# Kernel tuning notes

Hardware: AMD Instinct MI355X
Metric: run time of the kernel (lower is better)

The kernel has to match this reference:

```python
import jax, jax.numpy as jnp
import numpy as np

POS_THR = 0.5      # ROI_POSITIVE_THR
NEG_THR = 0.1      # ROI_NEGATIVE_THR
N_SAMPLES = 256    # ROI_SAMPLES
FG_RATIO = 0.25    # ROI_SAMPLE_RATIO
L1W = 1.0          # RPN.L1WEIGHT_INTERSECTION
NUM_FG = int(N_SAMPLES * FG_RATIO)


def _make_boxes(kxy, kwh, shape):
    # valid [x1,y1,x2,y2] boxes in an ~800px image
    xy = jax.random.uniform(kxy, shape[:-1] + (2,)) * 800.0
    wh = jax.random.uniform(kwh, shape[:-1] + (2,)) * 200.0 + 1.0
    return jnp.concatenate([xy, xy + wh], axis=-1)


def setup_inputs() -> dict:
    key = jax.random.key(0)
    k1, k2, k3, k4 = jax.random.split(key, 4)
    proposals = _make_boxes(k1, k2, (16, 16384, 4))  # [B, N, 4]
    gt_boxes = _make_boxes(k3, k4, (16, 128, 4))     # [B, G, 4]
    return {"proposals": proposals, "gt_boxes": gt_boxes}


def _centrehw(b):
    # [x1,y1,x2,y2] -> [cx,cy,w,h]
    x1, y1, x2, y2 = b[..., 0], b[..., 1], b[..., 2], b[..., 3]
    return jnp.stack([(x1 + x2) * 0.5, (y1 + y2) * 0.5, x2 - x1, y2 - y1], axis=-1)


def _targets(gt_c, roi_c):
    dx = (gt_c[..., 0] - roi_c[..., 0]) / roi_c[..., 2]
    dy = (gt_c[..., 1] - roi_c[..., 1]) / roi_c[..., 3]
    dw = jnp.log(gt_c[..., 2] / roi_c[..., 2])
    dh = jnp.log(gt_c[..., 3] / roi_c[..., 3])
    return jnp.stack([dx, dy, dw, dh], axis=-1)


def _iou(prop, gt):
    # prop [B,N,4], gt [B,G,4] -> IoU [B,N,G]
    p = prop[:, :, None, :]
    g = gt[:, None, :, :]
    ix1 = jnp.maximum(p[..., 0], g[..., 0])
    iy1 = jnp.maximum(p[..., 1], g[..., 1])
    ix2 = jnp.minimum(p[..., 2], g[..., 2])
    iy2 = jnp.minimum(p[..., 3], g[..., 3])
    inter = jnp.clip(ix2 - ix1, 0.0) * jnp.clip(iy2 - iy1, 0.0)
    ap = (p[..., 2] - p[..., 0]) * (p[..., 3] - p[..., 1])
    ag = (g[..., 2] - g[..., 0]) * (g[..., 3] - g[..., 1])
    return inter / jnp.maximum(ap + ag - inter, 1e-8)


def _forward(proposals, gt_boxes):
    B, N, _ = proposals.shape
    iou = _iou(proposals, gt_boxes)                       # [B,N,G]
    max_iou = iou.max(axis=-1)                            # [B,N]
    argmax_gt = iou.argmax(axis=-1).astype(jnp.int32)     # [B,N]
    # classify: 1=fg, 0=bg, -1=ignore
    labels = jnp.where(max_iou >= POS_THR, 1,
                       jnp.where(max_iou < NEG_THR, 0, -1)).astype(jnp.int32)
    # randsample: keep <= NUM_FG positives (random), fill rest with negatives.
    r = jax.random.uniform(jax.random.key(1), (B, N))
    pos = labels == 1
    r_pos = jnp.where(pos, r, -1.0)
    order = jnp.argsort(-r_pos, axis=1)
    ranks = jnp.argsort(order, axis=1)                    # rank among positives by r
    pos_sel = pos & (ranks < NUM_FG)
    prio = jnp.where(pos_sel, 3.0 + r,
                     jnp.where(labels == 0, 2.0 + r,
                               jnp.where(pos, 1.0 + r, r)))
    _, idx = jax.lax.top_k(prio, N_SAMPLES)               # [B,S] sampled proposal ids
    batch_labels = jnp.maximum(jnp.take_along_axis(labels, idx, axis=1), 0)  # [B,S]
    roi_batch = jnp.take_along_axis(proposals, idx[..., None], axis=1)       # [B,S,4]
    sel_gt = jnp.take_along_axis(argmax_gt, idx, axis=1)                     # [B,S]
    gt_batch = jnp.take_along_axis(gt_boxes, sel_gt[..., None], axis=1)      # [B,S,4]
    bbox_targets = _targets(_centrehw(gt_batch), _centrehw(roi_batch))       # [B,S,4]
    in_w = jnp.where((batch_labels == 1)[..., None], L1W, 0.0)
    in_w = jnp.broadcast_to(in_w, bbox_targets.shape)
    out_w = (in_w > 0).astype(jnp.float32)
    return roi_batch, batch_labels, bbox_targets, in_w, out_w


def reference(proposals, gt_boxes):
    return _forward(proposals, gt_boxes)
```

## Files before the change

kernel.cpp:

```cpp
#include <hip/hip_runtime.h>
#include <stdint.h>

#define BATCH 16
#define NPROP 16384
#define NGT   128
#define NSAMP 256
#define NFG   64
#define GCAP  512
#define CSTR  128
#define NEGT  0x780002u

typedef unsigned long long ull;

__device__ __forceinline__ void thr_block(uint32_t c0, uint32_t c1,
                                          uint32_t* o0, uint32_t* o1) {
    const uint32_t k0 = 0u, k1 = 1u, ks2 = 0x1BD11BDBu;
    uint32_t x0 = c0 + k0, x1 = c1 + k1;
#define RND(d) { x0 += x1; x1 = (x1 << d) | (x1 >> (32 - d)); x1 ^= x0; }
    RND(13) RND(15) RND(26) RND(6)   x0 += k1;  x1 += ks2 + 1u;
    RND(17) RND(29) RND(16) RND(24)  x0 += ks2; x1 += k0 + 2u;
    RND(13) RND(15) RND(26) RND(6)   x0 += k0;  x1 += k1 + 3u;
    RND(17) RND(29) RND(16) RND(24)  x0 += k1;  x1 += ks2 + 4u;
    RND(13) RND(15) RND(26) RND(6)   x0 += ks2; x1 += k0 + 5u;
#undef RND
    *o0 = x0; *o1 = x1;
}

__device__ __forceinline__ uint32_t thr_part_xor(uint32_t f) {
    uint32_t a, b; thr_block(0u, f, &a, &b);
    return a ^ b;
}

__global__ void k_zero(uint32_t* c) {
    for (int i = threadIdx.x; i < BATCH * CSTR; i += 1024) c[i] = 0u;
}

__global__ void __launch_bounds__(256) k_compute(
    const float* __restrict__ props, const float* __restrict__ gts,
    ull* __restrict__ lists, uint32_t* __restrict__ cnts)
{
#pragma clang fp contract(off)
    const int b = blockIdx.y;
    const int tid = threadIdx.x;
    const int half = tid & 1;
    const int n = blockIdx.x * 128 + (tid >> 1);
    __shared__ float2 sA[130];
    __shared__ float2 sB[130];
    __shared__ float  sag[130];
    __shared__ uint32_t wc[4][4];
    __shared__ uint32_t we[4][4];
    __shared__ uint32_t sBase[4];
    if (tid < NGT) {
        float4 g = ((const float4*)gts)[(size_t)b * NGT + tid];
        int idx = (tid < 64) ? tid : tid + 1;
        sA[idx] = make_float2(g.x, g.y);
        sB[idx] = make_float2(g.z, g.w);
        sag[idx] = (g.z - g.x) * (g.w - g.y);
    }
    __syncthreads();
    const float4 pb = ((const float4*)props)[(size_t)b * NPROP + n];
    const float ap = (pb.z - pb.x) * (pb.w - pb.y);
    float best = -1.0f; int bg = 0;
    const int base  = half ? 65 : 0;
    const int gbias = half ? 64 : 0;
    #pragma unroll 4
    for (int i = 0; i < 64; ++i) {
        const float2 a = sA[base + i];
        const float2 c = sB[base + i];
        float w  = fmaxf(fminf(pb.z, c.x) - fmaxf(pb.x, a.x), 0.0f);
        float hh = fmaxf(fminf(pb.w, c.y) - fmaxf(pb.y, a.y), 0.0f);
        float inter = w * hh;
        float un = fmaxf(ap + sag[base + i] - inter, 1e-8f);
        float iou = inter / un;
        if (iou > best) { best = iou; bg = gbias + i; }
    }
    float ob = __shfl_xor(best, 1);
    int  obg = __shfl_xor(bg, 1);
    if (half == 0 && ob > best) { best = ob; bg = obg; }

    uint32_t lab = (best >= 0.5f) ? 2u : ((best < 0.1f) ? 1u : 0u);
    const uint32_t f = (uint32_t)b * NPROP + (uint32_t)n;
    uint32_t mant = thr_part_xor(f) >> 9;
    ull entry = ((ull)(lab == 2u) << 44) | ((ull)mant << 21)
              | ((ull)(16383u - (uint32_t)n) << 7) | (ull)(uint32_t)bg;

    const bool isEven = (half == 0);
    bool cP = isEven && (lab == 2u);
    bool cH = isEven && (lab == 1u) && (mant >= NEGT);
    bool cL = isEven && (lab == 1u) && (mant <  NEGT);
    bool cI = isEven && (lab == 0u);
    ull mP = __ballot(cP), mH = __ballot(cH), mL = __ballot(cL), mI = __ballot(cI);
    const int w = tid >> 6;
    const uint32_t lane = (uint32_t)tid & 63u;
    if (lane == 0) {
        wc[0][w] = (uint32_t)__popcll(mP);
        wc[1][w] = (uint32_t)__popcll(mH);
        wc[2][w] = (uint32_t)__popcll(mL);
        wc[3][w] = (uint32_t)__popcll(mI);
    }
    __syncthreads();
    if (tid < 4) {
        uint32_t e = 0;
        #pragma unroll
        for (int i = 0; i < 4; i++) { we[tid][i] = e; e += wc[tid][i]; }
        sBase[tid] = e ? atomicAdd(&cnts[b * CSTR + tid * 32], e) : 0u;
    }
    __syncthreads();
    ull lt = lane ? (~0ull >> (64u - lane)) : 0ull;
    ull* slab = lists + ((size_t)b * 4) * NPROP;
    if (cP) slab[0 * NPROP + sBase[0] + we[0][w] + (uint32_t)__popcll(mP & lt)] = entry;
    if (cH) slab[1 * NPROP + sBase[1] + we[1][w] + (uint32_t)__popcll(mH & lt)] = entry;
    if (cL) slab[2 * NPROP + sBase[2] + we[2][w] + (uint32_t)__popcll(mL & lt)] = entry;
    if (cI) slab[3 * NPROP + sBase[3] + we[3][w] + (uint32_t)__popcll(mI & lt)] = entry;
}

__global__ void __launch_bounds__(1024) k_select(
    const float* __restrict__ props, const float* __restrict__ gts,
    const ull* __restrict__ lists, const uint32_t* __restrict__ cnts,
    float* __restrict__ out)
{
#pragma clang fp contract(off)
    const int b = blockIdx.x;
    const int tid = threadIdx.x;
    __shared__ uint32_t hist[2048];
    __shared__ ull      gat[GCAP];
    __shared__ ull      selk[NSAMP];
    __shared__ uint32_t sela[NSAMP];
    __shared__ uint32_t sh_dig, sh_k, sh_cnt_in, gcnt, selc;
    __shared__ ull sh_thr;

    const ull* Ppos  = lists + ((size_t)b * 4 + 0) * NPROP;
    const ull* PnegH = lists + ((size_t)b * 4 + 1) * NPROP;
    const ull* PnegL = lists + ((size_t)b * 4 + 2) * NPROP;
    const ull* Pign  = lists + ((size_t)b * 4 + 3) * NPROP;
    const uint32_t npos = cnts[b * CSTR + 0];
    const uint32_t nH   = cnts[b * CSTR + 32];
    const uint32_t nL   = cnts[b * CSTR + 64];
    const uint32_t nig  = cnts[b * CSTR + 96];
    const uint32_t nneg = nH + nL;
    const uint32_t npn  = npos + nneg;
    if (tid == 0) selc = 0;
    __syncthreads();

    auto keyA_of = [](ull e) -> ull {
        return (((e >> 21) & 0x7FFFFFull) << 14) | ((e >> 7) & 0x3FFFull);
    };

    auto locate = [&](uint32_t k) {
        if (tid < 64) {
            const uint32_t lane = (uint32_t)tid;
            uint32_t cs = 0;
            if (lane < 32) {
                const uint32_t base = lane * 64u;
                #pragma unroll 8
                for (uint32_t i = 0; i < 64; i++) cs += hist[base + i];
            }
            uint32_t s = cs;
            #pragma unroll
            for (int off = 1; off < 32; off <<= 1) {
                uint32_t t = __shfl_down(s, off);
                if (lane + off < 32) s += t;
            }
            uint32_t sExcl = s - cs;
            bool cond = (lane < 32) && (sExcl < k) && (k <= s);
            ull ball = __ballot(cond);
            uint32_t cstar = (uint32_t)(__ffsll((unsigned long long)ball) - 1);
            uint32_t kc = (uint32_t)__shfl((int)(k - sExcl), (int)cstar);
            uint32_t val = hist[cstar * 64u + lane];
            uint32_t fi = val;
            #pragma unroll
            for (int off = 1; off < 64; off <<= 1) {
                uint32_t t = __shfl_down(fi, off);
                if (lane + off < 64) fi += t;
            }
            uint32_t fExcl = fi - val;
            bool cond2 = (fExcl < kc) && (kc <= fi);
            ull ball2 = __ballot(cond2);
            uint32_t bstar = (uint32_t)(__ffsll((unsigned long long)ball2) - 1);
            if (lane == bstar) {
                sh_dig = cstar * 64u + lane;
                sh_k = kc - fExcl;
                sh_cnt_in = val;
            }
        }
    };

    auto radix = [&](auto&& kf, uint32_t m, uint32_t k, int shift) -> ull {
        if (m <= GCAP) {
            if (tid == 0) gcnt = 0;
            __syncthreads();
            for (uint32_t j = tid; j < m; j += 1024) {
                bool e; ull key = kf(j, e);
                if (e) { uint32_t s = atomicAdd(&gcnt, 1u); gat[s] = key; }
            }
            __syncthreads();
            uint32_t gc = gcnt;
            if (tid < (int)gc) {
                ull x = gat[tid];
                uint32_t r = 0;
                for (uint32_t j = 0; j < gc; j++) r += (gat[j] > x);
                if (r == k - 1) sh_thr = x;
            }
            __syncthreads();
            return sh_thr;
        }
        ull prefix = 0, mask = 0;
        for (;;) {
            hist[tid] = 0; hist[tid + 1024] = 0;
            __syncthreads();
            for (uint32_t j = tid; j < m; j += 1024) {
                bool e; ull key = kf(j, e);
                if (e && ((key ^ prefix) & mask) == 0)
                    atomicAdd(&hist[(uint32_t)(key >> shift) & 2047u], 1u);
            }
            __syncthreads();
            locate(k);
            __syncthreads();
            uint32_t dig = sh_dig, kk = sh_k, cnt = sh_cnt_in;
            prefix |= ((ull)dig) << shift;
            mask   |= 2047ull << shift;
            if (cnt <= GCAP || shift == 0) {
                if (tid == 0) gcnt = 0;
                __syncthreads();
                for (uint32_t j = tid; j < m; j += 1024) {
                    bool e; ull key = kf(j, e);
                    if (e && ((key ^ prefix) & mask) == 0) {
                        uint32_t s = atomicAdd(&gcnt, 1u);
                        if (s < GCAP) gat[s] = key;
                    }
                }
                __syncthreads();
                uint32_t gc = (gcnt < GCAP) ? gcnt : GCAP;
                if (tid < (int)gc) {
                    ull x = gat[tid];
                    uint32_t r = 0;
                    for (uint32_t j = 0; j < gc; j++) r += (gat[j] > x);
                    if (r == kk - 1) sh_thr = x;
                }
                __syncthreads();
                return sh_thr;
            } else {
                k = kk;
                shift = (shift >= 11) ? shift - 11 : 0;
                __syncthreads();
            }
        }
    };

    ull thrA = 0;
    if (npos > NFG) {
        thrA = radix([&](uint32_t j, bool& e) -> ull {
            e = true; return keyA_of(Ppos[j]); }, npos, NFG, 26);
    }

    auto keyB_pos = [&](ull ent) -> ull {
        uint32_t mant = (uint32_t)((ent >> 21) & 0x7FFFFFull);
        uint32_t invn = (uint32_t)((ent >> 7) & 0x3FFFull);
        float r = __uint_as_float(0x3F800000u | mant) - 1.0f;
        uint32_t cls = (keyA_of(ent) >= thrA) ? 3u : 1u;
        float prio = (float)cls + r;
        return (((ull)__float_as_uint(prio)) << 14) | (ull)invn;
    };
    auto keyB_neg = [](ull ent) -> ull {
        uint32_t mant = (uint32_t)((ent >> 21) & 0x7FFFFFull);
        uint32_t invn = (uint32_t)((ent >> 7) & 0x3FFFull);
        float r = __uint_as_float(0x3F800000u | mant) - 1.0f;
        float prio = 2.0f + r;
        return (((ull)__float_as_uint(prio)) << 14) | (ull)invn;
    };
    auto keyB_ign = [](ull ent) -> ull {
        uint32_t mant = (uint32_t)((ent >> 21) & 0x7FFFFFull);
        uint32_t invn = (uint32_t)((ent >> 7) & 0x3FFFull);
        float r = __uint_as_float(0x3F800000u | mant) - 1.0f;
        float prio = 0.0f + r;
        return (((ull)__float_as_uint(prio)) << 14) | (ull)invn;
    };

    const uint32_t c3 = (npos < NFG) ? npos : NFG;
    const uint32_t c2 = nneg;
    uint32_t clsStar = (npn >= NSAMP) ? ((NSAMP <= c3 + c2) ? 2u : 1u) : 0u;
    bool scanL = true;
    const bool scanI = (clsStar == 0u);
    ull thrB = 0;
    if (clsStar == 2u) {
        uint32_t k2 = NSAMP - c3;
        if (nH >= k2) {
            scanL = false;
            thrB = radix([&](uint32_t j, bool& e) -> ull {
                e = true; return keyB_neg(PnegH[j]); }, nH, k2, 25);
        } else {
            thrB = radix([&](uint32_t j, bool& e) -> ull {
                e = true; return keyB_neg(j < nH ? PnegH[j] : PnegL[j - nH]); },
                nneg, k2, 25);
        }
    } else if (clsStar == 1u) {
        uint32_t k1 = NSAMP - c3 - c2;
        thrB = radix([&](uint32_t j, bool& e) -> ull {
            ull kb = keyB_pos(Ppos[j]);
            e = ((kb >> 14) < 0x40000000ull);
            return kb; }, npos, k1, 26);
    } else {
        uint32_t k0 = NSAMP - npn;
        thrB = radix([&](uint32_t j, bool& e) -> ull {
            e = true; return keyB_ign(Pign[j]); }, nig, k0, 34);
    }
    __syncthreads();

    auto push = [&](ull key, ull ent, uint32_t fg) {
        uint32_t s = atomicAdd(&selc, 1u);
        if (s < NSAMP) { selk[s] = key; sela[s] = (fg << 7) | (uint32_t)(ent & 0x7Full); }
    };
    for (uint32_t j = tid; j < npos; j += 1024) {
        ull ent = Ppos[j]; ull key = keyB_pos(ent);
        if (clsStar == 0u || key >= thrB) push(key, ent, 1u);
    }
    for (uint32_t j = tid; j < nH; j += 1024) {
        ull ent = PnegH[j]; ull key = keyB_neg(ent);
        if (clsStar == 0u || key >= thrB) push(key, ent, 0u);
    }
    if (scanL) {
        for (uint32_t j = tid; j < nL; j += 1024) {
            ull ent = PnegL[j]; ull key = keyB_neg(ent);
            if (clsStar == 0u || key >= thrB) push(key, ent, 0u);
        }
    }
    if (scanI) {
        for (uint32_t j = tid; j < nig; j += 1024) {
            ull ent = Pign[j]; ull key = keyB_ign(ent);
            if (key >= thrB) push(key, ent, 0u);
        }
    }
    __syncthreads();

    if (tid < NSAMP) {
        ull x = selk[tid];
        uint32_t r = 0;
        for (int j = 0; j < NSAMP; j++) r += (selk[j] > x);
        uint32_t n = 16383u - (uint32_t)((x >> 0) & 0x3FFFull);
        uint32_t aux = sela[tid];
        uint32_t bg = aux & 0x7Fu;
        const int isfg = (int)((aux >> 7) & 1u);
        const float4 pb = ((const float4*)props)[(size_t)b * NPROP + n];
        const float4 gb = ((const float4*)gts)[(size_t)b * NGT + bg];
        const size_t O_ROI = 0;
        const size_t O_LBL = (size_t)BATCH * NSAMP * 4;
        const size_t O_TGT = O_LBL + (size_t)BATCH * NSAMP;
        const size_t O_INW = O_TGT + (size_t)BATCH * NSAMP * 4;
        const size_t O_OUW = O_INW + (size_t)BATCH * NSAMP * 4;
        const size_t row = (size_t)b * NSAMP + r;
        out[O_ROI + row * 4 + 0] = pb.x;
        out[O_ROI + row * 4 + 1] = pb.y;
        out[O_ROI + row * 4 + 2] = pb.z;
        out[O_ROI + row * 4 + 3] = pb.w;
        out[O_LBL + row] = isfg ? 1.0f : 0.0f;
        float rw  = pb.z - pb.x, rh = pb.w - pb.y;
        float gw  = gb.z - gb.x, gh = gb.w - gb.y;
        out[O_TGT + row * 4 + 0] = ((gb.x + gb.z) * 0.5f - (pb.x + pb.z) * 0.5f) / rw;
        out[O_TGT + row * 4 + 1] = ((gb.y + gb.w) * 0.5f - (pb.y + pb.w) * 0.5f) / rh;
        out[O_TGT + row * 4 + 2] = logf(gw / rw);
        out[O_TGT + row * 4 + 3] = logf(gh / rh);
        float wv = isfg ? 1.0f : 0.0f;
        for (int c = 0; c < 4; c++) {
            out[O_INW + row * 4 + c] = wv;
            out[O_OUW + row * 4 + c] = wv;
        }
    }
}

extern "C" void kernel_launch(void* const* d_in, const int* in_sizes, int n_in,
                              void* d_out, int out_size, void* d_ws, size_t ws_size,
                              hipStream_t stream) {
    (void)in_sizes; (void)n_in; (void)out_size; (void)ws_size;
    const float* props = (const float*)d_in[0];
    const float* gts   = (const float*)d_in[1];
    ull* lists = (ull*)d_ws;
    uint32_t* cnts = (uint32_t*)((char*)d_ws + (size_t)BATCH * 4 * NPROP * 8);
    float* out = (float*)d_out;

    k_zero<<<1, 1024, 0, stream>>>(cnts);
    dim3 gridA(NPROP / 128, BATCH);
    k_compute<<<gridA, 256, 0, stream>>>(props, gts, lists, cnts);
    k_select<<<BATCH, 1024, 0, stream>>>(props, gts, lists, cnts, out);
}
```

Before: 96.23 us.

## Skip non-overlapping IoU divisions, use per-block segments instead of global atomics

```diff
diff --git a/kernel.cpp b/kernel.cpp
--- a/kernel.cpp
+++ b/kernel.cpp
@@ -7,8 +7,10 @@
 #define NSAMP 256
 #define NFG   64
 #define GCAP  512
-#define CSTR  128
-#define NEGT  0x780002u
+#define PCAP  8192
+#define NCAP  4096
+#define NBLK  128
+#define BPB   128
 
 typedef unsigned long long ull;
 
@@ -31,25 +33,20 @@
     return a ^ b;
 }
 
-__global__ void k_zero(uint32_t* c) {
-    for (int i = threadIdx.x; i < BATCH * CSTR; i += 1024) c[i] = 0u;
-}
-
 __global__ void __launch_bounds__(256) k_compute(
     const float* __restrict__ props, const float* __restrict__ gts,
-    ull* __restrict__ lists, uint32_t* __restrict__ cnts)
+    ull* __restrict__ lists, uint32_t* __restrict__ cntblk)
 {
 #pragma clang fp contract(off)
     const int b = blockIdx.y;
+    const int blk = blockIdx.x;
     const int tid = threadIdx.x;
     const int half = tid & 1;
-    const int n = blockIdx.x * 128 + (tid >> 1);
+    const int n = blk * BPB + (tid >> 1);
     __shared__ float2 sA[130];
     __shared__ float2 sB[130];
     __shared__ float  sag[130];
-    __shared__ uint32_t wc[4][4];
-    __shared__ uint32_t we[4][4];
-    __shared__ uint32_t sBase[4];
+    __shared__ uint32_t wc[3][4], we_s[3][4];
     if (tid < NGT) {
         float4 g = ((const float4*)gts)[(size_t)b * NGT + tid];
         int idx = (tid < 64) ? tid : tid + 1;
@@ -60,11 +57,30 @@
     __syncthreads();
     const float4 pb = ((const float4*)props)[(size_t)b * NPROP + n];
     const float ap = (pb.z - pb.x) * (pb.w - pb.y);
-    float best = -1.0f; int bg = 0;
     const int base  = half ? 65 : 0;
     const int gbias = half ? 64 : 0;
+
+    uint32_t m0 = 0, m1 = 0;
     #pragma unroll 4
-    for (int i = 0; i < 64; ++i) {
+    for (int i = 0; i < 32; ++i) {
+        const float2 a = sA[base + i];
+        const float2 c = sB[base + i];
+        uint32_t hit = (fminf(pb.z, c.x) > fmaxf(pb.x, a.x)) &
+                       (fminf(pb.w, c.y) > fmaxf(pb.y, a.y));
+        m0 |= hit << i;
+    }
+    #pragma unroll 4
+    for (int i = 0; i < 32; ++i) {
+        const float2 a = sA[base + 32 + i];
+        const float2 c = sB[base + 32 + i];
+        uint32_t hit = (fminf(pb.z, c.x) > fmaxf(pb.x, a.x)) &
+                       (fminf(pb.w, c.y) > fmaxf(pb.y, a.y));
+        m1 |= hit << i;
+    }
+
+    float best = 0.0f; int bg = gbias;
+    while (m0) {
+        int i = __builtin_ctz(m0); m0 &= m0 - 1;
         const float2 a = sA[base + i];
         const float2 c = sB[base + i];
         float w  = fmaxf(fminf(pb.z, c.x) - fmaxf(pb.x, a.x), 0.0f);
@@ -74,6 +90,18 @@
         float iou = inter / un;
         if (iou > best) { best = iou; bg = gbias + i; }
     }
+    while (m1) {
+        int i = 32 + __builtin_ctz(m1); m1 &= m1 - 1;
+        const float2 a = sA[base + i];
+        const float2 c = sB[base + i];
+        float w  = fmaxf(fminf(pb.z, c.x) - fmaxf(pb.x, a.x), 0.0f);
+        float hh = fmaxf(fminf(pb.w, c.y) - fmaxf(pb.y, a.y), 0.0f);
+        float inter = w * hh;
+        float un = fmaxf(ap + sag[base + i] - inter, 1e-8f);
+        float iou = inter / un;
+        if (iou > best) { best = iou; bg = gbias + i; }
+    }
+
     float ob = __shfl_xor(best, 1);
     int  obg = __shfl_xor(bg, 1);
     if (half == 0 && ob > best) { best = ob; bg = obg; }
@@ -86,61 +114,90 @@
 
     const bool isEven = (half == 0);
     bool cP = isEven && (lab == 2u);
-    bool cH = isEven && (lab == 1u) && (mant >= NEGT);
-    bool cL = isEven && (lab == 1u) && (mant <  NEGT);
+    bool cN = isEven && (lab == 1u);
     bool cI = isEven && (lab == 0u);
-    ull mP = __ballot(cP), mH = __ballot(cH), mL = __ballot(cL), mI = __ballot(cI);
+    ull mP = __ballot(cP), mN = __ballot(cN), mI = __ballot(cI);
     const int w = tid >> 6;
     const uint32_t lane = (uint32_t)tid & 63u;
     if (lane == 0) {
         wc[0][w] = (uint32_t)__popcll(mP);
-        wc[1][w] = (uint32_t)__popcll(mH);
-        wc[2][w] = (uint32_t)__popcll(mL);
-        wc[3][w] = (uint32_t)__popcll(mI);
-    }
-    __syncthreads();
-    if (tid < 4) {
+        wc[1][w] = (uint32_t)__popcll(mN);
+        wc[2][w] = (uint32_t)__popcll(mI);
+    }
+    __syncthreads();
+    if (tid < 3) {
         uint32_t e = 0;
         #pragma unroll
-        for (int i = 0; i < 4; i++) { we[tid][i] = e; e += wc[tid][i]; }
-        sBase[tid] = e ? atomicAdd(&cnts[b * CSTR + tid * 32], e) : 0u;
+        for (int i = 0; i < 4; i++) { we_s[tid][i] = e; e += wc[tid][i]; }
+        cntblk[((size_t)b * NBLK + blk) * 4 + tid] = e;
     }
     __syncthreads();
     ull lt = lane ? (~0ull >> (64u - lane)) : 0ull;
-    ull* slab = lists + ((size_t)b * 4) * NPROP;
-    if (cP) slab[0 * NPROP + sBase[0] + we[0][w] + (uint32_t)__popcll(mP & lt)] = entry;
-    if (cH) slab[1 * NPROP + sBase[1] + we[1][w] + (uint32_t)__popcll(mH & lt)] = entry;
-    if (cL) slab[2 * NPROP + sBase[2] + we[2][w] + (uint32_t)__popcll(mL & lt)] = entry;
-    if (cI) slab[3 * NPROP + sBase[3] + we[3][w] + (uint32_t)__popcll(mI & lt)] = entry;
+    ull* slab = lists + (size_t)b * 3 * NPROP;
+    const uint32_t segB = (uint32_t)blk * BPB;
+    if (cP) slab[0 * NPROP + segB + we_s[0][w] + (uint32_t)__popcll(mP & lt)] = entry;
+    if (cN) slab[1 * NPROP + segB + we_s[1][w] + (uint32_t)__popcll(mN & lt)] = entry;
+    if (cI) slab[2 * NPROP + segB + we_s[2][w] + (uint32_t)__popcll(mI & lt)] = entry;
 }
 
 __global__ void __launch_bounds__(1024) k_select(
     const float* __restrict__ props, const float* __restrict__ gts,
-    const ull* __restrict__ lists, const uint32_t* __restrict__ cnts,
+    const ull* __restrict__ lists, const uint32_t* __restrict__ cntblk,
     float* __restrict__ out)
 {
 #pragma clang fp contract(off)
     const int b = blockIdx.x;
     const int tid = threadIdx.x;
+    __shared__ ull      dpos[PCAP];
+    __shared__ ull      dneg[NCAP];
     __shared__ uint32_t hist[2048];
     __shared__ ull      gat[GCAP];
     __shared__ ull      selk[NSAMP];
     __shared__ uint32_t sela[NSAMP];
+    __shared__ uint32_t bc[NBLK * 4];
+    __shared__ uint32_t preP[NBLK], preN[NBLK];
     __shared__ uint32_t sh_dig, sh_k, sh_cnt_in, gcnt, selc;
+    __shared__ uint32_t totP, totN, totI;
     __shared__ ull sh_thr;
 
-    const ull* Ppos  = lists + ((size_t)b * 4 + 0) * NPROP;
-    const ull* PnegH = lists + ((size_t)b * 4 + 1) * NPROP;
-    const ull* PnegL = lists + ((size_t)b * 4 + 2) * NPROP;
-    const ull* Pign  = lists + ((size_t)b * 4 + 3) * NPROP;
-    const uint32_t npos = cnts[b * CSTR + 0];
-    const uint32_t nH   = cnts[b * CSTR + 32];
-    const uint32_t nL   = cnts[b * CSTR + 64];
-    const uint32_t nig  = cnts[b * CSTR + 96];
-    const uint32_t nneg = nH + nL;
-    const uint32_t npn  = npos + nneg;
+    const ull* Spos = lists + (size_t)b * 3 * NPROP;
+    const ull* Sneg = Spos + NPROP;
+    const ull* Sign = Sneg + NPROP;
+    if (tid < NBLK * 4) bc[tid] = cntblk[(size_t)b * NBLK * 4 + tid];
     if (tid == 0) selc = 0;
     __syncthreads();
+    if (tid < 3) {
+        uint32_t run = 0;
+        for (int blk = 0; blk < NBLK; ++blk) {
+            uint32_t v = bc[blk * 4 + tid];
+            if (tid == 0) preP[blk] = run;
+            else if (tid == 1) preN[blk] = run;
+            run += v;
+        }
+        if (tid == 0) totP = run; else if (tid == 1) totN = run; else totI = run;
+    }
+    __syncthreads();
+    const uint32_t npos = totP, nneg = totN, nig = totI;
+    const bool posL = (npos <= PCAP), negL = (nneg <= NCAP);
+    for (uint32_t s = tid; s < NPROP; s += 1024) {
+        uint32_t blk = s >> 7, i = s & 127u;
+        if (posL && i < bc[blk * 4 + 0]) dpos[preP[blk] + i] = Spos[s];
+        if (negL && i < bc[blk * 4 + 1]) dneg[preN[blk] + i] = Sneg[s];
+    }
+    __syncthreads();
+
+    const uint32_t mPos = posL ? npos : NPROP;
+    const uint32_t mNeg = negL ? nneg : NPROP;
+    auto posEnt = [&](uint32_t j, bool& e) -> ull {
+        if (posL) { e = true; return dpos[j]; }
+        e = (j & 127u) < bc[(j >> 7) * 4 + 0];
+        return e ? Spos[j] : 0ull;
+    };
+    auto negEnt = [&](uint32_t j, bool& e) -> ull {
+        if (negL) { e = true; return dneg[j]; }
+        e = (j & 127u) < bc[(j >> 7) * 4 + 1];
+        return e ? Sneg[j] : 0ull;
+    };
 
     auto keyA_of = [](ull e) -> ull {
         return (((e >> 21) & 0x7FFFFFull) << 14) | ((e >> 7) & 0x3FFFull);
@@ -250,7 +307,7 @@
     ull thrA = 0;
     if (npos > NFG) {
         thrA = radix([&](uint32_t j, bool& e) -> ull {
-            e = true; return keyA_of(Ppos[j]); }, npos, NFG, 26);
+            ull ent = posEnt(j, e); return keyA_of(ent); }, mPos, NFG, 26);
     }
 
     auto keyB_pos = [&](ull ent) -> ull {
@@ -278,31 +335,22 @@
 
     const uint32_t c3 = (npos < NFG) ? npos : NFG;
     const uint32_t c2 = nneg;
+    const uint32_t npn = npos + nneg;
     uint32_t clsStar = (npn >= NSAMP) ? ((NSAMP <= c3 + c2) ? 2u : 1u) : 0u;
-    bool scanL = true;
-    const bool scanI = (clsStar == 0u);
     ull thrB = 0;
     if (clsStar == 2u) {
-        uint32_t k2 = NSAMP - c3;
-        if (nH >= k2) {
-            scanL = false;
-            thrB = radix([&](uint32_t j, bool& e) -> ull {
-                e = true; return keyB_neg(PnegH[j]); }, nH, k2, 25);
-        } else {
-            thrB = radix([&](uint32_t j, bool& e) -> ull {
-                e = true; return keyB_neg(j < nH ? PnegH[j] : PnegL[j - nH]); },
-                nneg, k2, 25);
-        }
+        thrB = radix([&](uint32_t j, bool& e) -> ull {
+            ull ent = negEnt(j, e); return keyB_neg(ent); }, mNeg, NSAMP - c3, 26);
     } else if (clsStar == 1u) {
-        uint32_t k1 = NSAMP - c3 - c2;
         thrB = radix([&](uint32_t j, bool& e) -> ull {
-            ull kb = keyB_pos(Ppos[j]);
-            e = ((kb >> 14) < 0x40000000ull);
-            return kb; }, npos, k1, 26);
+            ull ent = posEnt(j, e);
+            ull kb = keyB_pos(ent);
+            e = e && ((kb >> 14) < 0x40000000ull);
+            return kb; }, mPos, NSAMP - c3 - c2, 26);
     } else {
-        uint32_t k0 = NSAMP - npn;
         thrB = radix([&](uint32_t j, bool& e) -> ull {
-            e = true; return keyB_ign(Pign[j]); }, nig, k0, 34);
+            e = (j & 127u) < bc[(j >> 7) * 4 + 2];
+            return e ? keyB_ign(Sign[j]) : 0ull; }, NPROP, NSAMP - npn, 34);
     }
     __syncthreads();
 
@@ -310,24 +358,25 @@
         uint32_t s = atomicAdd(&selc, 1u);
         if (s < NSAMP) { selk[s] = key; sela[s] = (fg << 7) | (uint32_t)(ent & 0x7Full); }
     };
-    for (uint32_t j = tid; j < npos; j += 1024) {
-        ull ent = Ppos[j]; ull key = keyB_pos(ent);
+    for (uint32_t j = tid; j < mPos; j += 1024) {
+        bool e; ull ent = posEnt(j, e);
+        if (!e) continue;
+        ull key = keyB_pos(ent);
         if (clsStar == 0u || key >= thrB) push(key, ent, 1u);
     }
-    for (uint32_t j = tid; j < nH; j += 1024) {
-        ull ent = PnegH[j]; ull key = keyB_neg(ent);
+    for (uint32_t j = tid; j < mNeg; j += 1024) {
+        bool e; ull ent = negEnt(j, e);
+        if (!e) continue;
+        ull key = keyB_neg(ent);
         if (clsStar == 0u || key >= thrB) push(key, ent, 0u);
     }
-    if (scanL) {
-        for (uint32_t j = tid; j < nL; j += 1024) {
-            ull ent = PnegL[j]; ull key = keyB_neg(ent);
-            if (clsStar == 0u || key >= thrB) push(key, ent, 0u);
-        }
-    }
-    if (scanI) {
-        for (uint32_t j = tid; j < nig; j += 1024) {
-            ull ent = Pign[j]; ull key = keyB_ign(ent);
-            if (key >= thrB) push(key, ent, 0u);
+    if (clsStar == 0u) {
+        for (uint32_t j = tid; j < NPROP; j += 1024) {
+            if (((j & 127u) < bc[(j >> 7) * 4 + 2])) {
+                ull ent = Sign[j];
+                ull key = keyB_ign(ent);
+                if (key >= thrB) push(key, ent, 0u);
+            }
         }
     }
     __syncthreads();
@@ -336,7 +385,7 @@
         ull x = selk[tid];
         uint32_t r = 0;
         for (int j = 0; j < NSAMP; j++) r += (selk[j] > x);
-        uint32_t n = 16383u - (uint32_t)((x >> 0) & 0x3FFFull);
+        uint32_t n = 16383u - (uint32_t)(x & 0x3FFFull);
         uint32_t aux = sela[tid];
         uint32_t bg = aux & 0x7Fu;
         const int isfg = (int)((aux >> 7) & 1u);
@@ -374,11 +423,10 @@
     const float* props = (const float*)d_in[0];
     const float* gts   = (const float*)d_in[1];
     ull* lists = (ull*)d_ws;
-    uint32_t* cnts = (uint32_t*)((char*)d_ws + (size_t)BATCH * 4 * NPROP * 8);
+    uint32_t* cntblk = (uint32_t*)((char*)d_ws + (size_t)BATCH * 3 * NPROP * 8);
     float* out = (float*)d_out;
 
-    k_zero<<<1, 1024, 0, stream>>>(cnts);
-    dim3 gridA(NPROP / 128, BATCH);
-    k_compute<<<gridA, 256, 0, stream>>>(props, gts, lists, cnts);
-    k_select<<<BATCH, 1024, 0, stream>>>(props, gts, lists, cnts, out);
+    dim3 gridA(NPROP / BPB, BATCH);
+    k_compute<<<gridA, 256, 0, stream>>>(props, gts, lists, cntblk);
+    k_select<<<BATCH, 1024, 0, stream>>>(props, gts, lists, cntblk, out);
 }
```

Result: slower. 109.4 us (+13.7%).

## Fuse IoU/bucketing and selection into one persistent kernel with grid barrier

Applied to the files above, without the earlier changes.

```diff
diff --git a/kernel.cpp b/kernel.cpp
--- a/kernel.cpp
+++ b/kernel.cpp
@@ -7,7 +7,7 @@
 #define NSAMP 256
 #define NFG   64
 #define GCAP  512
-#define CSTR  128
+#define PCAP  8192
 #define NEGT  0x780002u
 
 typedef unsigned long long ull;
@@ -31,97 +31,25 @@
     return a ^ b;
 }
 
-__global__ void k_zero(uint32_t* c) {
-    for (int i = threadIdx.x; i < BATCH * CSTR; i += 1024) c[i] = 0u;
+__global__ void k_init(uint32_t* z) {
+    if (threadIdx.x < 16 * 8 * 2 + 2) z[threadIdx.x] = 0u;
 }
 
-__global__ void __launch_bounds__(256) k_compute(
+__global__ void __launch_bounds__(1024, 4) k_fused(
     const float* __restrict__ props, const float* __restrict__ gts,
-    ull* __restrict__ lists, uint32_t* __restrict__ cnts)
+    ull* __restrict__ lists, ull* __restrict__ cnts, uint32_t* __restrict__ bar,
+    float* __restrict__ out)
 {
 #pragma clang fp contract(off)
-    const int b = blockIdx.y;
     const int tid = threadIdx.x;
-    const int half = tid & 1;
-    const int n = blockIdx.x * 128 + (tid >> 1);
+    const int bid = blockIdx.x;
+
     __shared__ float2 sA[130];
     __shared__ float2 sB[130];
     __shared__ float  sag[130];
-    __shared__ uint32_t wc[4][4];
-    __shared__ uint32_t we[4][4];
-    __shared__ uint32_t sBase[4];
-    if (tid < NGT) {
-        float4 g = ((const float4*)gts)[(size_t)b * NGT + tid];
-        int idx = (tid < 64) ? tid : tid + 1;
-        sA[idx] = make_float2(g.x, g.y);
-        sB[idx] = make_float2(g.z, g.w);
-        sag[idx] = (g.z - g.x) * (g.w - g.y);
-    }
-    __syncthreads();
-    const float4 pb = ((const float4*)props)[(size_t)b * NPROP + n];
-    const float ap = (pb.z - pb.x) * (pb.w - pb.y);
-    float best = -1.0f; int bg = 0;
-    const int base  = half ? 65 : 0;
-    const int gbias = half ? 64 : 0;
-    #pragma unroll 4
-    for (int i = 0; i < 64; ++i) {
-        const float2 a = sA[base + i];
-        const float2 c = sB[base + i];
-        float w  = fmaxf(fminf(pb.z, c.x) - fmaxf(pb.x, a.x), 0.0f);
-        float hh = fmaxf(fminf(pb.w, c.y) - fmaxf(pb.y, a.y), 0.0f);
-        float inter = w * hh;
-        float un = fmaxf(ap + sag[base + i] - inter, 1e-8f);
-        float iou = inter / un;
-        if (iou > best) { best = iou; bg = gbias + i; }
-    }
-    float ob = __shfl_xor(best, 1);
-    int  obg = __shfl_xor(bg, 1);
-    if (half == 0 && ob > best) { best = ob; bg = obg; }
-
-    uint32_t lab = (best >= 0.5f) ? 2u : ((best < 0.1f) ? 1u : 0u);
-    const uint32_t f = (uint32_t)b * NPROP + (uint32_t)n;
-    uint32_t mant = thr_part_xor(f) >> 9;
-    ull entry = ((ull)(lab == 2u) << 44) | ((ull)mant << 21)
-              | ((ull)(16383u - (uint32_t)n) << 7) | (ull)(uint32_t)bg;
-
-    const bool isEven = (half == 0);
-    bool cP = isEven && (lab == 2u);
-    bool cH = isEven && (lab == 1u) && (mant >= NEGT);
-    bool cL = isEven && (lab == 1u) && (mant <  NEGT);
-    bool cI = isEven && (lab == 0u);
-    ull mP = __ballot(cP), mH = __ballot(cH), mL = __ballot(cL), mI = __ballot(cI);
-    const int w = tid >> 6;
-    const uint32_t lane = (uint32_t)tid & 63u;
-    if (lane == 0) {
-        wc[0][w] = (uint32_t)__popcll(mP);
-        wc[1][w] = (uint32_t)__popcll(mH);
-        wc[2][w] = (uint32_t)__popcll(mL);
-        wc[3][w] = (uint32_t)__popcll(mI);
-    }
-    __syncthreads();
-    if (tid < 4) {
-        uint32_t e = 0;
-        #pragma unroll
-        for (int i = 0; i < 4; i++) { we[tid][i] = e; e += wc[tid][i]; }
-        sBase[tid] = e ? atomicAdd(&cnts[b * CSTR + tid * 32], e) : 0u;
-    }
-    __syncthreads();
-    ull lt = lane ? (~0ull >> (64u - lane)) : 0ull;
-    ull* slab = lists + ((size_t)b * 4) * NPROP;
-    if (cP) slab[0 * NPROP + sBase[0] + we[0][w] + (uint32_t)__popcll(mP & lt)] = entry;
-    if (cH) slab[1 * NPROP + sBase[1] + we[1][w] + (uint32_t)__popcll(mH & lt)] = entry;
-    if (cL) slab[2 * NPROP + sBase[2] + we[2][w] + (uint32_t)__popcll(mL & lt)] = entry;
-    if (cI) slab[3 * NPROP + sBase[3] + we[3][w] + (uint32_t)__popcll(mI & lt)] = entry;
-}
-
-__global__ void __launch_bounds__(1024) k_select(
-    const float* __restrict__ props, const float* __restrict__ gts,
-    const ull* __restrict__ lists, const uint32_t* __restrict__ cnts,
-    float* __restrict__ out)
-{
-#pragma clang fp contract(off)
-    const int b = blockIdx.x;
-    const int tid = threadIdx.x;
+    __shared__ uint32_t wc[4][16], we_s[4][16];
+    __shared__ ull sPack;
+    __shared__ ull      dpos[PCAP];
     __shared__ uint32_t hist[2048];
     __shared__ ull      gat[GCAP];
     __shared__ ull      selk[NSAMP];
@@ -129,19 +57,123 @@
     __shared__ uint32_t sh_dig, sh_k, sh_cnt_in, gcnt, selc;
     __shared__ ull sh_thr;
 
-    const ull* Ppos  = lists + ((size_t)b * 4 + 0) * NPROP;
-    const ull* PnegH = lists + ((size_t)b * 4 + 1) * NPROP;
-    const ull* PnegL = lists + ((size_t)b * 4 + 2) * NPROP;
-    const ull* Pign  = lists + ((size_t)b * 4 + 3) * NPROP;
-    const uint32_t npos = cnts[b * CSTR + 0];
-    const uint32_t nH   = cnts[b * CSTR + 32];
-    const uint32_t nL   = cnts[b * CSTR + 64];
-    const uint32_t nig  = cnts[b * CSTR + 96];
+    {
+        const int ab = bid >> 4;
+        const int half = tid & 1;
+        if (tid < NGT) {
+            float4 g = ((const float4*)gts)[(size_t)ab * NGT + tid];
+            int idx = (tid < 64) ? tid : tid + 1;
+            sA[idx] = make_float2(g.x, g.y);
+            sB[idx] = make_float2(g.z, g.w);
+            sag[idx] = (g.z - g.x) * (g.w - g.y);
+        }
+        __syncthreads();
+        const int base  = half ? 65 : 0;
+        const int gbias = half ? 64 : 0;
+        ull* slab = lists + (size_t)ab * 4 * NPROP;
+
+        for (int cc = 0; cc < 2; ++cc) {
+            const int seg = (bid & 15) * 2 + cc;
+            const int n = seg * 512 + (tid >> 1);
+            const float4 pb = ((const float4*)props)[(size_t)ab * NPROP + n];
+            const float ap = (pb.z - pb.x) * (pb.w - pb.y);
+            float best = -1.0f; int bg = 0;
+            #pragma unroll 4
+            for (int i = 0; i < 64; ++i) {
+                const float2 a = sA[base + i];
+                const float2 c = sB[base + i];
+                float w  = fmaxf(fminf(pb.z, c.x) - fmaxf(pb.x, a.x), 0.0f);
+                float hh = fmaxf(fminf(pb.w, c.y) - fmaxf(pb.y, a.y), 0.0f);
+                float inter = w * hh;
+                float un = fmaxf(ap + sag[base + i] - inter, 1e-8f);
+                float iou = inter / un;
+                if (iou > best) { best = iou; bg = gbias + i; }
+            }
+            float ob = __shfl_xor(best, 1);
+            int  obg = __shfl_xor(bg, 1);
+            if (half == 0 && ob > best) { best = ob; bg = obg; }
+
+            uint32_t lab = (best >= 0.5f) ? 2u : ((best < 0.1f) ? 1u : 0u);
+            const uint32_t f = (uint32_t)ab * NPROP + (uint32_t)n;
+            uint32_t mant = thr_part_xor(f) >> 9;
+            ull entry = ((ull)(lab == 2u) << 44) | ((ull)mant << 21)
+                      | ((ull)(16383u - (uint32_t)n) << 7) | (ull)(uint32_t)bg;
+
+            const bool isEven = (half == 0);
+            bool cP = isEven && (lab == 2u);
+            bool cH = isEven && (lab == 1u) && (mant >= NEGT);
+            bool cL = isEven && (lab == 1u) && (mant <  NEGT);
+            bool cI = isEven && (lab == 0u);
+            ull mP = __ballot(cP), mH = __ballot(cH), mL = __ballot(cL), mI = __ballot(cI);
+            const int w = tid >> 6;
+            const uint32_t lane = (uint32_t)tid & 63u;
+            if (lane == 0) {
+                wc[0][w] = (uint32_t)__popcll(mP);
+                wc[1][w] = (uint32_t)__popcll(mH);
+                wc[2][w] = (uint32_t)__popcll(mL);
+                wc[3][w] = (uint32_t)__popcll(mI);
+            }
+            __syncthreads();
+            if (tid < 4) {
+                uint32_t e = 0;
+                #pragma unroll
+                for (int i = 0; i < 16; i++) { we_s[tid][i] = e; e += wc[tid][i]; }
+                uint32_t e0 = (uint32_t)__shfl((int)e, 0);
+                uint32_t e1 = (uint32_t)__shfl((int)e, 1);
+                uint32_t e2 = (uint32_t)__shfl((int)e, 2);
+                uint32_t e3 = (uint32_t)__shfl((int)e, 3);
+                if (tid == 0) {
+                    ull add = (ull)e0 | ((ull)e1 << 16) | ((ull)e2 << 32) | ((ull)e3 << 48);
+                    sPack = atomicAdd(&cnts[(size_t)ab * 8], add);
+                }
+            }
+            __syncthreads();
+            ull pk = sPack;
+            uint32_t b0 = (uint32_t)(pk)       & 0xFFFFu;
+            uint32_t b1 = (uint32_t)(pk >> 16) & 0xFFFFu;
+            uint32_t b2 = (uint32_t)(pk >> 32) & 0xFFFFu;
+            uint32_t b3 = (uint32_t)(pk >> 48) & 0xFFFFu;
+            ull lt = lane ? (~0ull >> (64u - lane)) : 0ull;
+            if (cP) slab[0 * NPROP + b0 + we_s[0][w] + (uint32_t)__popcll(mP & lt)] = entry;
+            if (cH) slab[1 * NPROP + b1 + we_s[1][w] + (uint32_t)__popcll(mH & lt)] = entry;
+            if (cL) slab[2 * NPROP + b2 + we_s[2][w] + (uint32_t)__popcll(mL & lt)] = entry;
+            if (cI) slab[3 * NPROP + b3 + we_s[3][w] + (uint32_t)__popcll(mI & lt)] = entry;
+            __syncthreads();
+        }
+    }
+
+    __syncthreads();
+    if (tid == 0) {
+        __threadfence();
+        uint32_t arrived = atomicAdd(&bar[0], 1u) + 1u;
+        if (arrived == (uint32_t)gridDim.x) {
+            atomicExch(&bar[1], 1u);
+        } else {
+            while (atomicAdd(&bar[1], 0u) == 0u) __builtin_amdgcn_s_sleep(8);
+        }
+        __threadfence();
+    }
+    __syncthreads();
+    if (bid >= BATCH) return;
+
+    const int sb = bid;
+    const ull* Ppos  = lists + ((size_t)sb * 4 + 0) * NPROP;
+    const ull* PnegH = lists + ((size_t)sb * 4 + 1) * NPROP;
+    const ull* PnegL = lists + ((size_t)sb * 4 + 2) * NPROP;
+    const ull* Pign  = lists + ((size_t)sb * 4 + 3) * NPROP;
+    const ull pk = cnts[(size_t)sb * 8];
+    const uint32_t npos = (uint32_t)(pk)       & 0xFFFFu;
+    const uint32_t nH   = (uint32_t)(pk >> 16) & 0xFFFFu;
+    const uint32_t nL   = (uint32_t)(pk >> 32) & 0xFFFFu;
+    const uint32_t nig  = (uint32_t)(pk >> 48) & 0xFFFFu;
     const uint32_t nneg = nH + nL;
     const uint32_t npn  = npos + nneg;
+    const bool inP = (npos <= PCAP);
     if (tid == 0) selc = 0;
+    if (inP) for (uint32_t j = tid; j < npos; j += 1024) dpos[j] = Ppos[j];
     __syncthreads();
 
+    auto posEnt = [&](uint32_t j) -> ull { return inP ? dpos[j] : Ppos[j]; };
     auto keyA_of = [](ull e) -> ull {
         return (((e >> 21) & 0x7FFFFFull) << 14) | ((e >> 7) & 0x3FFFull);
     };
@@ -250,7 +282,7 @@
     ull thrA = 0;
     if (npos > NFG) {
         thrA = radix([&](uint32_t j, bool& e) -> ull {
-            e = true; return keyA_of(Ppos[j]); }, npos, NFG, 26);
+            e = true; return keyA_of(posEnt(j)); }, npos, NFG, 26);
     }
 
     auto keyB_pos = [&](ull ent) -> ull {
@@ -287,22 +319,20 @@
         if (nH >= k2) {
             scanL = false;
             thrB = radix([&](uint32_t j, bool& e) -> ull {
-                e = true; return keyB_neg(PnegH[j]); }, nH, k2, 25);
+                e = true; return keyB_neg(PnegH[j]); }, nH, k2, 26);
         } else {
             thrB = radix([&](uint32_t j, bool& e) -> ull {
                 e = true; return keyB_neg(j < nH ? PnegH[j] : PnegL[j - nH]); },
-                nneg, k2, 25);
+                nneg, k2, 26);
         }
     } else if (clsStar == 1u) {
-        uint32_t k1 = NSAMP - c3 - c2;
         thrB = radix([&](uint32_t j, bool& e) -> ull {
-            ull kb = keyB_pos(Ppos[j]);
+            ull kb = keyB_pos(posEnt(j));
             e = ((kb >> 14) < 0x40000000ull);
-            return kb; }, npos, k1, 26);
+            return kb; }, npos, NSAMP - c3 - c2, 26);
     } else {
-        uint32_t k0 = NSAMP - npn;
         thrB = radix([&](uint32_t j, bool& e) -> ull {
-            e = true; return keyB_ign(Pign[j]); }, nig, k0, 34);
+            e = true; return keyB_ign(Pign[j]); }, nig, NSAMP - npn, 34);
     }
     __syncthreads();
 
@@ -311,7 +341,7 @@
         if (s < NSAMP) { selk[s] = key; sela[s] = (fg << 7) | (uint32_t)(ent & 0x7Full); }
     };
     for (uint32_t j = tid; j < npos; j += 1024) {
-        ull ent = Ppos[j]; ull key = keyB_pos(ent);
+        ull ent = posEnt(j); ull key = keyB_pos(ent);
         if (clsStar == 0u || key >= thrB) push(key, ent, 1u);
     }
     for (uint32_t j = tid; j < nH; j += 1024) {
@@ -336,18 +366,18 @@
         ull x = selk[tid];
         uint32_t r = 0;
         for (int j = 0; j < NSAMP; j++) r += (selk[j] > x);
-        uint32_t n = 16383u - (uint32_t)((x >> 0) & 0x3FFFull);
+        uint32_t n = 16383u - (uint32_t)(x & 0x3FFFull);
         uint32_t aux = sela[tid];
         uint32_t bg = aux & 0x7Fu;
         const int isfg = (int)((aux >> 7) & 1u);
-        const float4 pb = ((const float4*)props)[(size_t)b * NPROP + n];
-        const float4 gb = ((const float4*)gts)[(size_t)b * NGT + bg];
+        const float4 pb = ((const float4*)props)[(size_t)sb * NPROP + n];
+        const float4 gb = ((const float4*)gts)[(size_t)sb * NGT + bg];
         const size_t O_ROI = 0;
         const size_t O_LBL = (size_t)BATCH * NSAMP * 4;
         const size_t O_TGT = O_LBL + (size_t)BATCH * NSAMP;
         const size_t O_INW = O_TGT + (size_t)BATCH * NSAMP * 4;
         const size_t O_OUW = O_INW + (size_t)BATCH * NSAMP * 4;
-        const size_t row = (size_t)b * NSAMP + r;
+        const size_t row = (size_t)sb * NSAMP + r;
         out[O_ROI + row * 4 + 0] = pb.x;
         out[O_ROI + row * 4 + 1] = pb.y;
         out[O_ROI + row * 4 + 2] = pb.z;
@@ -374,11 +404,10 @@
     const float* props = (const float*)d_in[0];
     const float* gts   = (const float*)d_in[1];
     ull* lists = (ull*)d_ws;
-    uint32_t* cnts = (uint32_t*)((char*)d_ws + (size_t)BATCH * 4 * NPROP * 8);
+    ull* cnts  = (ull*)((char*)d_ws + (size_t)BATCH * 4 * NPROP * 8);
+    uint32_t* bar = (uint32_t*)(cnts + BATCH * 8);
     float* out = (float*)d_out;
 
-    k_zero<<<1, 1024, 0, stream>>>(cnts);
-    dim3 gridA(NPROP / 128, BATCH);
-    k_compute<<<gridA, 256, 0, stream>>>(props, gts, lists, cnts);
-    k_select<<<BATCH, 1024, 0, stream>>>(props, gts, lists, cnts, out);
+    k_init<<<1, 512, 0, stream>>>((uint32_t*)cnts);
+    k_fused<<<256, 1024, 0, stream>>>(props, gts, lists, cnts, bar, out);
 }
```

Result: slower. 119.5 us (+24.2%).

## Replace global atomic list append with per-block segments and LDS compaction

Applied to the files above, without the earlier changes.

```diff
diff --git a/kernel.cpp b/kernel.cpp
--- a/kernel.cpp
+++ b/kernel.cpp
@@ -7,7 +7,10 @@
 #define NSAMP 256
 #define NFG   64
 #define GCAP  512
-#define CSTR  128
+#define PCAP  8192
+#define HCAP  2048
+#define NBLK  128
+#define BPB   128
 #define NEGT  0x780002u
 
 typedef unsigned long long ull;
@@ -31,25 +34,20 @@
     return a ^ b;
 }
 
-__global__ void k_zero(uint32_t* c) {
-    for (int i = threadIdx.x; i < BATCH * CSTR; i += 1024) c[i] = 0u;
-}
-
 __global__ void __launch_bounds__(256) k_compute(
     const float* __restrict__ props, const float* __restrict__ gts,
-    ull* __restrict__ lists, uint32_t* __restrict__ cnts)
+    ull* __restrict__ lists, uint32_t* __restrict__ cntblk)
 {
 #pragma clang fp contract(off)
     const int b = blockIdx.y;
+    const int blk = blockIdx.x;
     const int tid = threadIdx.x;
     const int half = tid & 1;
-    const int n = blockIdx.x * 128 + (tid >> 1);
+    const int n = blk * BPB + (tid >> 1);
     __shared__ float2 sA[130];
     __shared__ float2 sB[130];
     __shared__ float  sag[130];
-    __shared__ uint32_t wc[4][4];
-    __shared__ uint32_t we[4][4];
-    __shared__ uint32_t sBase[4];
+    __shared__ uint32_t wc[4][4], we_s[4][4];
     if (tid < NGT) {
         float4 g = ((const float4*)gts)[(size_t)b * NGT + tid];
         int idx = (tid < 64) ? tid : tid + 1;
@@ -102,45 +100,106 @@
     if (tid < 4) {
         uint32_t e = 0;
         #pragma unroll
-        for (int i = 0; i < 4; i++) { we[tid][i] = e; e += wc[tid][i]; }
-        sBase[tid] = e ? atomicAdd(&cnts[b * CSTR + tid * 32], e) : 0u;
+        for (int i = 0; i < 4; i++) { we_s[tid][i] = e; e += wc[tid][i]; }
+        cntblk[((size_t)b * NBLK + blk) * 4 + tid] = e;
     }
     __syncthreads();
     ull lt = lane ? (~0ull >> (64u - lane)) : 0ull;
-    ull* slab = lists + ((size_t)b * 4) * NPROP;
-    if (cP) slab[0 * NPROP + sBase[0] + we[0][w] + (uint32_t)__popcll(mP & lt)] = entry;
-    if (cH) slab[1 * NPROP + sBase[1] + we[1][w] + (uint32_t)__popcll(mH & lt)] = entry;
-    if (cL) slab[2 * NPROP + sBase[2] + we[2][w] + (uint32_t)__popcll(mL & lt)] = entry;
-    if (cI) slab[3 * NPROP + sBase[3] + we[3][w] + (uint32_t)__popcll(mI & lt)] = entry;
+    ull* slab = lists + (size_t)b * 4 * NPROP;
+    const uint32_t segB = (uint32_t)blk * BPB;
+    if (cP) slab[0 * NPROP + segB + we_s[0][w] + (uint32_t)__popcll(mP & lt)] = entry;
+    if (cH) slab[1 * NPROP + segB + we_s[1][w] + (uint32_t)__popcll(mH & lt)] = entry;
+    if (cL) slab[2 * NPROP + segB + we_s[2][w] + (uint32_t)__popcll(mL & lt)] = entry;
+    if (cI) slab[3 * NPROP + segB + we_s[3][w] + (uint32_t)__popcll(mI & lt)] = entry;
 }
 
 __global__ void __launch_bounds__(1024) k_select(
     const float* __restrict__ props, const float* __restrict__ gts,
-    const ull* __restrict__ lists, const uint32_t* __restrict__ cnts,
+    const ull* __restrict__ lists, const uint32_t* __restrict__ cntblk,
     float* __restrict__ out)
 {
 #pragma clang fp contract(off)
     const int b = blockIdx.x;
     const int tid = threadIdx.x;
+    const int wid = tid >> 6;
+    const uint32_t lane = (uint32_t)tid & 63u;
+    __shared__ ull      dpos[PCAP];
+    __shared__ ull      dnh[HCAP];
     __shared__ uint32_t hist[2048];
     __shared__ ull      gat[GCAP];
     __shared__ ull      selk[NSAMP];
     __shared__ uint32_t sela[NSAMP];
-    __shared__ uint32_t sh_dig, sh_k, sh_cnt_in, gcnt, selc;
+    __shared__ uint32_t bc[NBLK * 4];
+    __shared__ uint32_t tot[4];
+    __shared__ uint32_t sh_dig, sh_k, sh_cnt_in, gcnt, selc, stP, stH;
     __shared__ ull sh_thr;
 
-    const ull* Ppos  = lists + ((size_t)b * 4 + 0) * NPROP;
-    const ull* PnegH = lists + ((size_t)b * 4 + 1) * NPROP;
-    const ull* PnegL = lists + ((size_t)b * 4 + 2) * NPROP;
-    const ull* Pign  = lists + ((size_t)b * 4 + 3) * NPROP;
-    const uint32_t npos = cnts[b * CSTR + 0];
-    const uint32_t nH   = cnts[b * CSTR + 32];
-    const uint32_t nL   = cnts[b * CSTR + 64];
-    const uint32_t nig  = cnts[b * CSTR + 96];
+    const ull* Spos = lists + ((size_t)b * 4 + 0) * NPROP;
+    const ull* SnH  = lists + ((size_t)b * 4 + 1) * NPROP;
+    const ull* SnL  = lists + ((size_t)b * 4 + 2) * NPROP;
+    const ull* Sign = lists + ((size_t)b * 4 + 3) * NPROP;
+    if (tid < 4) tot[tid] = 0;
+    if (tid == 0) { selc = 0; stP = 0; stH = 0; }
+    __syncthreads();
+    if (tid < NBLK * 4) {
+        uint32_t v = cntblk[(size_t)b * NBLK * 4 + tid];
+        bc[tid] = v;
+        atomicAdd(&tot[tid & 3], v);
+    }
+    __syncthreads();
+    const uint32_t npos = tot[0], nH = tot[1], nL = tot[2], nig = tot[3];
     const uint32_t nneg = nH + nL;
     const uint32_t npn  = npos + nneg;
-    if (tid == 0) selc = 0;
-    __syncthreads();
+    const bool dP = (npos <= PCAP), dH = (nH <= HCAP);
+
+    {
+        for (int s8 = 0; s8 < 8; ++s8) {
+            uint32_t seg = (uint32_t)(wid * 8 + s8);
+            if (dP) {
+                uint32_t c = bc[seg * 4 + 0];
+                for (uint32_t i0 = 0; i0 < c; i0 += 64) {
+                    uint32_t take = (c - i0 < 64u) ? (c - i0) : 64u;
+                    uint32_t s0 = 0;
+                    if (lane == 0) s0 = atomicAdd(&stP, take);
+                    s0 = (uint32_t)__shfl((int)s0, 0);
+                    if (lane < take) dpos[s0 + lane] = Spos[seg * BPB + i0 + lane];
+                }
+            }
+            if (dH) {
+                uint32_t c = bc[seg * 4 + 1];
+                for (uint32_t i0 = 0; i0 < c; i0 += 64) {
+                    uint32_t take = (c - i0 < 64u) ? (c - i0) : 64u;
+                    uint32_t s0 = 0;
+                    if (lane == 0) s0 = atomicAdd(&stH, take);
+                    s0 = (uint32_t)__shfl((int)s0, 0);
+                    if (lane < take) dnh[s0 + lane] = SnH[seg * BPB + i0 + lane];
+                }
+            }
+        }
+    }
+    __syncthreads();
+
+    const uint32_t MSEG = NBLK * BPB;
+    const uint32_t mPos = dP ? npos : MSEG;
+    const uint32_t mH   = dH ? nH   : MSEG;
+    auto posEnt = [&](uint32_t j, bool& e) -> ull {
+        if (dP) { e = true; return dpos[j]; }
+        e = (j & (BPB - 1u)) < bc[(j >> 7) * 4 + 0];
+        return e ? Spos[j] : 0ull;
+    };
+    auto nhEnt = [&](uint32_t j, bool& e) -> ull {
+        if (dH) { e = true; return dnh[j]; }
+        e = (j & (BPB - 1u)) < bc[(j >> 7) * 4 + 1];
+        return e ? SnH[j] : 0ull;
+    };
+    auto nlEnt = [&](uint32_t j, bool& e) -> ull {
+        e = (j & (BPB - 1u)) < bc[(j >> 7) * 4 + 2];
+        return e ? SnL[j] : 0ull;
+    };
+    auto igEnt = [&](uint32_t j, bool& e) -> ull {
+        e = (j & (BPB - 1u)) < bc[(j >> 7) * 4 + 3];
+        return e ? Sign[j] : 0ull;
+    };
 
     auto keyA_of = [](ull e) -> ull {
         return (((e >> 21) & 0x7FFFFFull) << 14) | ((e >> 7) & 0x3FFFull);
@@ -148,12 +207,12 @@
 
     auto locate = [&](uint32_t k) {
         if (tid < 64) {
-            const uint32_t lane = (uint32_t)tid;
             uint32_t cs = 0;
             if (lane < 32) {
                 const uint32_t base = lane * 64u;
                 #pragma unroll 8
-                for (uint32_t i = 0; i < 64; i++) cs += hist[base + i];
+                for (uint32_t i = 0; i < 64; i++)
+                    cs += hist[base + ((i + lane) & 63u)];
             }
             uint32_t s = cs;
             #pragma unroll
@@ -250,7 +309,7 @@
     ull thrA = 0;
     if (npos > NFG) {
         thrA = radix([&](uint32_t j, bool& e) -> ull {
-            e = true; return keyA_of(Ppos[j]); }, npos, NFG, 26);
+            ull ent = posEnt(j, e); return keyA_of(ent); }, mPos, NFG, 26);
     }
 
     auto keyB_pos = [&](ull ent) -> ull {
@@ -287,22 +346,22 @@
         if (nH >= k2) {
             scanL = false;
             thrB = radix([&](uint32_t j, bool& e) -> ull {
-                e = true; return keyB_neg(PnegH[j]); }, nH, k2, 25);
+                ull ent = nhEnt(j, e); return keyB_neg(ent); }, mH, k2, 26);
         } else {
             thrB = radix([&](uint32_t j, bool& e) -> ull {
-                e = true; return keyB_neg(j < nH ? PnegH[j] : PnegL[j - nH]); },
-                nneg, k2, 25);
+                if (j < mH) { ull ent = nhEnt(j, e); return keyB_neg(ent); }
+                ull ent = nlEnt(j - mH, e); return keyB_neg(ent); },
+                mH + MSEG, k2, 26);
         }
     } else if (clsStar == 1u) {
-        uint32_t k1 = NSAMP - c3 - c2;
         thrB = radix([&](uint32_t j, bool& e) -> ull {
-            ull kb = keyB_pos(Ppos[j]);
-            e = ((kb >> 14) < 0x40000000ull);
-            return kb; }, npos, k1, 26);
+            ull ent = posEnt(j, e);
+            ull kb = keyB_pos(ent);
+            e = e && ((kb >> 14) < 0x40000000ull);
+            return kb; }, mPos, NSAMP - c3 - c2, 26);
     } else {
-        uint32_t k0 = NSAMP - npn;
         thrB = radix([&](uint32_t j, bool& e) -> ull {
-            e = true; return keyB_ign(Pign[j]); }, nig, k0, 34);
+            ull ent = igEnt(j, e); return keyB_ign(ent); }, MSEG, NSAMP - npn, 34);
     }
     __syncthreads();
 
@@ -310,23 +369,31 @@
         uint32_t s = atomicAdd(&selc, 1u);
         if (s < NSAMP) { selk[s] = key; sela[s] = (fg << 7) | (uint32_t)(ent & 0x7Full); }
     };
-    for (uint32_t j = tid; j < npos; j += 1024) {
-        ull ent = Ppos[j]; ull key = keyB_pos(ent);
+    for (uint32_t j = tid; j < mPos; j += 1024) {
+        bool e; ull ent = posEnt(j, e);
+        if (!e) continue;
+        ull key = keyB_pos(ent);
         if (clsStar == 0u || key >= thrB) push(key, ent, 1u);
     }
-    for (uint32_t j = tid; j < nH; j += 1024) {
-        ull ent = PnegH[j]; ull key = keyB_neg(ent);
+    for (uint32_t j = tid; j < mH; j += 1024) {
+        bool e; ull ent = nhEnt(j, e);
+        if (!e) continue;
+        ull key = keyB_neg(ent);
         if (clsStar == 0u || key >= thrB) push(key, ent, 0u);
     }
     if (scanL) {
-        for (uint32_t j = tid; j < nL; j += 1024) {
-            ull ent = PnegL[j]; ull key = keyB_neg(ent);
+        for (uint32_t j = tid; j < MSEG; j += 1024) {
+            bool e; ull ent = nlEnt(j, e);
+            if (!e) continue;
+            ull key = keyB_neg(ent);
             if (clsStar == 0u || key >= thrB) push(key, ent, 0u);
         }
     }
     if (scanI) {
-        for (uint32_t j = tid; j < nig; j += 1024) {
-            ull ent = Pign[j]; ull key = keyB_ign(ent);
+        for (uint32_t j = tid; j < MSEG; j += 1024) {
+            bool e; ull ent = igEnt(j, e);
+            if (!e) continue;
+            ull key = keyB_ign(ent);
             if (key >= thrB) push(key, ent, 0u);
         }
     }
@@ -336,7 +403,7 @@
         ull x = selk[tid];
         uint32_t r = 0;
         for (int j = 0; j < NSAMP; j++) r += (selk[j] > x);
-        uint32_t n = 16383u - (uint32_t)((x >> 0) & 0x3FFFull);
+        uint32_t n = 16383u - (uint32_t)(x & 0x3FFFull);
         uint32_t aux = sela[tid];
         uint32_t bg = aux & 0x7Fu;
         const int isfg = (int)((aux >> 7) & 1u);
@@ -374,11 +441,10 @@
     const float* props = (const float*)d_in[0];
     const float* gts   = (const float*)d_in[1];
     ull* lists = (ull*)d_ws;
-    uint32_t* cnts = (uint32_t*)((char*)d_ws + (size_t)BATCH * 4 * NPROP * 8);
+    uint32_t* cntblk = (uint32_t*)((char*)d_ws + (size_t)BATCH * 4 * NPROP * 8);
     float* out = (float*)d_out;
 
-    k_zero<<<1, 1024, 0, stream>>>(cnts);
-    dim3 gridA(NPROP / 128, BATCH);
-    k_compute<<<gridA, 256, 0, stream>>>(props, gts, lists, cnts);
-    k_select<<<BATCH, 1024, 0, stream>>>(props, gts, lists, cnts, out);
+    dim3 gridA(NBLK, BATCH);
+    k_compute<<<gridA, 256, 0, stream>>>(props, gts, lists, cntblk);
+    k_select<<<BATCH, 1024, 0, stream>>>(props, gts, lists, cntblk, out);
 }
```

New measurement: 103.9 us. +8.0%, slower.
